# Kernel optimization log

Measured on AMD Instinct MI355X. Metric: run time of the kernel, lower is better.

The kernel has to match this reference:

```python
import jax, jax.numpy as jnp
import numpy as np

N_NODES = 50000
N_GRAPHS = 50
MAX_NODES = 1000  # equal-size graphs
C_IN = 128
C_OUT = 128
N_EDGES = 800000
N_LAYERS = 3
BN_EPS = 1e-5


def setup_inputs() -> dict:
    key = jax.random.key(0)
    ks = jax.random.split(key, 20)
    x = jax.random.normal(ks[0], (N_NODES, C_IN), dtype=jnp.float32)
    edge_index = jax.random.randint(ks[1], (2, N_EDGES), 0, N_NODES, dtype=jnp.int64)
    batch = jnp.repeat(jnp.arange(N_GRAPHS, dtype=jnp.int64), MAX_NODES)
    s_in = 1.0 / np.sqrt(C_IN)
    s_out = 1.0 / np.sqrt(C_OUT)
    fh_W = jax.random.normal(ks[2], (C_IN, C_OUT), dtype=jnp.float32) * s_in
    fh_b = jnp.zeros((C_OUT,), dtype=jnp.float32)
    W1 = jax.random.normal(ks[3], (N_LAYERS, C_OUT, C_OUT), dtype=jnp.float32) * s_out
    b1 = jnp.zeros((N_LAYERS, C_OUT), dtype=jnp.float32)
    g1 = jnp.ones((N_LAYERS, C_OUT), dtype=jnp.float32)
    be1 = jnp.zeros((N_LAYERS, C_OUT), dtype=jnp.float32)
    W2 = jax.random.normal(ks[4], (N_LAYERS, C_OUT, C_OUT), dtype=jnp.float32) * s_out
    b2 = jnp.zeros((N_LAYERS, C_OUT), dtype=jnp.float32)
    g2 = jnp.ones((N_LAYERS, C_OUT), dtype=jnp.float32)
    be2 = jnp.zeros((N_LAYERS, C_OUT), dtype=jnp.float32)
    return {"x": x, "edge_index": edge_index, "batch": batch,
            "fh_W": fh_W, "fh_b": fh_b,
            "W1": W1, "b1": b1, "g1": g1, "be1": be1,
            "W2": W2, "b2": b2, "g2": g2, "be2": be2}


def _bn(h, gamma, beta):
    # training-mode BatchNorm1d over the node dim (biased variance, like torch)
    mu = jnp.mean(h, axis=0)
    var = jnp.var(h, axis=0)
    return (h - mu) * jax.lax.rsqrt(var + BN_EPS) * gamma + beta


def _mlp(h, W1, b1, g1, be1, W2, b2, g2, be2):
    h = jax.nn.relu(_bn(h @ W1 + b1, g1, be1))
    h = jax.nn.relu(_bn(h @ W2 + b2, g2, be2))
    return h


def _to_dense_batch(h, batch):
    # counts per graph -> exclusive starts -> intra-graph position
    ones = jnp.ones((h.shape[0],), dtype=jnp.int32)
    counts = jax.ops.segment_sum(ones, batch, num_segments=N_GRAPHS)
    starts = jnp.cumsum(counts) - counts
    pos = jnp.arange(h.shape[0], dtype=jnp.int32) - starts[batch]
    dense = jnp.zeros((N_GRAPHS, MAX_NODES, h.shape[1]), dtype=h.dtype)
    return dense.at[batch, pos].set(h)


def reference(x, edge_index, batch, fh_W, fh_b, W1, b1, g1, be1, W2, b2, g2, be2):
    src, dst = edge_index[0], edge_index[1]
    h = x @ fh_W + fh_b  # first_head Linear
    outs = [_to_dense_batch(h, batch)]
    for l in range(N_LAYERS):
        # GINConv: mlp((1+eps)*x + sum_{j->i} x_j), eps=0
        agg = jax.ops.segment_sum(h[src], dst, num_segments=N_NODES)
        h = _mlp(h + agg, W1[l], b1[l], g1[l], be1[l], W2[l], b2[l], g2[l], be2[l])
        outs.append(_to_dense_batch(h, batch))
    return jnp.stack(outs)  # [N_LAYERS+1, B, MAX_NODES, C]
```

## Files before the change

### kernel.cpp

```cpp
#include <hip/hip_runtime.h>

#define NN 50000
#define NE 800000
#define CC 128
#define SLAB (NN * CC)
#define BN_EPS 1e-5f

typedef __attribute__((ext_vector_type(8))) short bf16x8;
typedef __attribute__((ext_vector_type(4))) float f32x4;
typedef unsigned short ushort_t;
typedef unsigned int uint_t;

__device__ inline ushort_t f2bf(float v) {
  unsigned u = __builtin_bit_cast(unsigned, v);
  unsigned r = u + 0x7FFFu + ((u >> 16) & 1u);
  return (ushort_t)(r >> 16);
}
__device__ inline float bf2f(unsigned lo16) { return __builtin_bit_cast(float, lo16 << 16); }

__global__ void zero_int_kernel(int* __restrict__ p, int n) {
  int i = blockIdx.x * blockDim.x + threadIdx.x;
  if (i < n) p[i] = 0;
}

__global__ void count_kernel(const int* __restrict__ dst, int* __restrict__ counts) {
  int e = blockIdx.x * blockDim.x + threadIdx.x;
  if (e < NE) atomicAdd(&counts[dst[e]], 1);
}

__global__ void scan1_kernel(const int* __restrict__ counts, int* __restrict__ excl,
                             int* __restrict__ blocksum) {
  __shared__ int s[256];
  int t = threadIdx.x;
  int i = blockIdx.x * 256 + t;
  int v = (i < NN) ? counts[i] : 0;
  s[t] = v;
  for (int off = 1; off < 256; off <<= 1) {
    __syncthreads();
    int add = (t >= off) ? s[t - off] : 0;
    __syncthreads();
    s[t] += add;
  }
  __syncthreads();
  if (i < NN) excl[i] = s[t] - v;
  if (t == 255) blocksum[blockIdx.x] = s[255];
}

__global__ void scan2_kernel(int* __restrict__ blocksum, int nb) {
  __shared__ int s[256];
  int t = threadIdx.x;
  int v = (t < nb) ? blocksum[t] : 0;
  s[t] = v;
  for (int off = 1; off < 256; off <<= 1) {
    __syncthreads();
    int add = (t >= off) ? s[t - off] : 0;
    __syncthreads();
    s[t] += add;
  }
  __syncthreads();
  if (t < nb) blocksum[t] = s[t] - v;
}

__global__ void scan3_kernel(int* __restrict__ excl, const int* __restrict__ blocksum) {
  int i = blockIdx.x * 256 + threadIdx.x;
  if (i < NN) excl[i] += blocksum[blockIdx.x];
}

__global__ void fill_kernel(const int* __restrict__ src, const int* __restrict__ dst,
                            const int* __restrict__ starts, int* __restrict__ fill,
                            int* __restrict__ bucket) {
  int e = blockIdx.x * blockDim.x + threadIdx.x;
  if (e < NE) {
    int d = dst[e];
    int pos = atomicAdd(&fill[d], 1);
    bucket[starts[d] + pos] = src[e];
  }
}

__global__ void prep_w_kernel(const float* __restrict__ fh_W, const float* __restrict__ W1,
                              const float* __restrict__ W2, short* __restrict__ whi,
                              short* __restrict__ wlo) {
  int m = blockIdx.x;
  const float* src = (m == 0) ? fh_W : ((m <= 3) ? W1 + (m - 1) * CC * CC : W2 + (m - 4) * CC * CC);
  short* hi = whi + m * CC * CC;
  short* lo = wlo + m * CC * CC;
  for (int it = 0; it < 64; ++it) {
    int idx = it * 256 + threadIdx.x;
    int j = idx & 7;
    int l = (idx >> 3) & 63;
    int nt = (idx >> 9) & 7;
    int ks = idx >> 12;
    int n = nt * 16 + (l & 15);
    int k = ks * 32 + ((l >> 4) << 3) + j;
    float v = src[k * CC + n];
    unsigned u = __builtin_bit_cast(unsigned, v);
    unsigned short h = (unsigned short)(u >> 16);
    float hf = __builtin_bit_cast(float, ((unsigned)h) << 16);
    float r = v - hf;
    unsigned ur = __builtin_bit_cast(unsigned, r);
    hi[idx] = (short)h;
    lo[idx] = (short)(ur >> 16);
  }
}

__global__ __launch_bounds__(256) void gemm0_kernel(
    const float* __restrict__ A, const short* __restrict__ Wp_hi, const short* __restrict__ Wp_lo,
    const float* __restrict__ bias, float* __restrict__ out, ushort_t* __restrict__ h16s) {
  const int t = threadIdx.x;
  const int l = t & 63;
  const int wv = t >> 6;
  const int m0 = blockIdx.x * 64 + wv * 16;
  const int row = m0 + (l & 15);
  const int kg = (l >> 4) * 8;

  f32x4 acc[8];
#pragma unroll
  for (int i = 0; i < 8; ++i) acc[i] = (f32x4){0.f, 0.f, 0.f, 0.f};

#pragma unroll
  for (int ks = 0; ks < 4; ++ks) {
    float av[8];
    if (row < NN) {
      const float* ap = &A[row * CC + ks * 32 + kg];
      float4 v0 = *(const float4*)ap;
      float4 v1 = *(const float4*)(ap + 4);
      av[0] = v0.x; av[1] = v0.y; av[2] = v0.z; av[3] = v0.w;
      av[4] = v1.x; av[5] = v1.y; av[6] = v1.z; av[7] = v1.w;
    } else {
#pragma unroll
      for (int i = 0; i < 8; ++i) av[i] = 0.f;
    }
    bf16x8 ah, al;
#pragma unroll
    for (int i = 0; i < 8; ++i) {
      unsigned u = __builtin_bit_cast(unsigned, av[i]);
      unsigned short hbits = (unsigned short)(u >> 16);
      float hf = __builtin_bit_cast(float, ((unsigned)hbits) << 16);
      float r = av[i] - hf;
      unsigned ur = __builtin_bit_cast(unsigned, r);
      ah[i] = (short)hbits;
      al[i] = (short)(ur >> 16);
    }
#pragma unroll
    for (int nt = 0; nt < 8; ++nt) {
      const int base = (ks * 8 + nt) * 512 + l * 8;
      bf16x8 wh = *(const bf16x8*)&Wp_hi[base];
      bf16x8 wl = *(const bf16x8*)&Wp_lo[base];
      acc[nt] = __builtin_amdgcn_mfma_f32_16x16x32_bf16(ah, wh, acc[nt], 0, 0, 0);
      acc[nt] = __builtin_amdgcn_mfma_f32_16x16x32_bf16(al, wh, acc[nt], 0, 0, 0);
      acc[nt] = __builtin_amdgcn_mfma_f32_16x16x32_bf16(ah, wl, acc[nt], 0, 0, 0);
    }
  }

  const int rbase = m0 + (l >> 4) * 4;
  const int cn = l & 15;
#pragma unroll
  for (int nt = 0; nt < 8; ++nt) {
    int c = nt * 16 + cn;
    float bv = bias[c];
#pragma unroll
    for (int r = 0; r < 4; ++r) {
      int rr = rbase + r;
      if (rr < NN) {
        float v = acc[nt][r] + bv;
        out[rr * CC + c] = v;
        h16s[(nt * NN + rr) * 16 + cn] = f2bf(v);
      }
    }
  }
}

__global__ __launch_bounds__(256) void gather_kernel(
    const ushort_t* __restrict__ h16s, const int* __restrict__ starts,
    const int* __restrict__ counts, const int* __restrict__ bucket,
    ushort_t* __restrict__ aggs) {
  const int slice = blockIdx.x & 7;
  const int t = threadIdx.x;
  const int g16 = t >> 4;
  const int lane16 = t & 15;
  const int j8 = lane16 & 7;
  const int half = lane16 >> 3;
  const int node = (blockIdx.x >> 3) * 16 + g16;
  const int wl_base = t & 48;
  const uint_t* tbl = (const uint_t*)h16s + slice * (NN * 8);

  float a0 = 0.f, a1 = 0.f;
  if (half == 0) {
    uint_t u = tbl[node * 8 + j8];
    a0 = bf2f(u & 0xFFFFu);
    a1 = bf2f(u >> 16);
  }
  const int s = starts[node];
  const int n = counts[node];
  for (int base = 0; base < n; base += 16) {
    int nb = n - base;
    if (nb > 16) nb = 16;
    int idx = (lane16 < nb) ? bucket[s + base + lane16] : -1;
#pragma unroll
    for (int k = 0; k < 8; ++k) {
      int sr = __shfl(idx, wl_base + 2 * k + half);
      if (sr >= 0) {
        uint_t u = tbl[sr * 8 + j8];
        a0 += bf2f(u & 0xFFFFu);
        a1 += bf2f(u >> 16);
      }
    }
  }
  a0 += __shfl_xor(a0, 8);
  a1 += __shfl_xor(a1, 8);
  if (half == 0) {
    ((uint_t*)aggs)[slice * (NN * 8) + node * 8 + j8] =
        (uint_t)f2bf(a0) | ((uint_t)f2bf(a1) << 16);
  }
}

__global__ __launch_bounds__(256) void gemm1_kernel(
    const ushort_t* __restrict__ aggs, const short* __restrict__ Wp_hi,
    const short* __restrict__ Wp_lo, const float* __restrict__ bias,
    ushort_t* __restrict__ tmp16, float* __restrict__ stats_out) {
  __shared__ float sred[2 * CC];
  const int t = threadIdx.x;
  const int l = t & 63;
  const int wv = t >> 6;
  const int m0 = blockIdx.x * 64 + wv * 16;
  const int row = m0 + (l & 15);
  const int kg = (l >> 4) * 8;
  sred[t] = 0.f;

  f32x4 acc[8];
#pragma unroll
  for (int i = 0; i < 8; ++i) acc[i] = (f32x4){0.f, 0.f, 0.f, 0.f};

#pragma unroll
  for (int ks = 0; ks < 4; ++ks) {
    const int ch0 = ks * 32 + kg;
    bf16x8 ah;
    if (row < NN) {
      ah = *(const bf16x8*)&aggs[((ch0 >> 4) * NN + row) * 16 + (ch0 & 15)];
    } else {
#pragma unroll
      for (int i = 0; i < 8; ++i) ah[i] = 0;
    }
#pragma unroll
    for (int nt = 0; nt < 8; ++nt) {
      const int base = (ks * 8 + nt) * 512 + l * 8;
      bf16x8 wh = *(const bf16x8*)&Wp_hi[base];
      bf16x8 wl = *(const bf16x8*)&Wp_lo[base];
      acc[nt] = __builtin_amdgcn_mfma_f32_16x16x32_bf16(ah, wh, acc[nt], 0, 0, 0);
      acc[nt] = __builtin_amdgcn_mfma_f32_16x16x32_bf16(ah, wl, acc[nt], 0, 0, 0);
    }
  }

  __syncthreads();
  const int rbase = m0 + (l >> 4) * 4;
  const int cn = l & 15;
#pragma unroll
  for (int nt = 0; nt < 8; ++nt) {
    int c = nt * 16 + cn;
    float bv = bias[c];
    float s = 0.f, qq = 0.f;
#pragma unroll
    for (int r = 0; r < 4; ++r) {
      int rr = rbase + r;
      if (rr < NN) {
        float v = acc[nt][r] + bv;
        tmp16[rr * CC + c] = f2bf(v);
        s += v; qq += v * v;
      }
    }
    s += __shfl_xor(s, 16); s += __shfl_xor(s, 32);
    qq += __shfl_xor(qq, 16); qq += __shfl_xor(qq, 32);
    if ((l >> 4) == 0) {
      atomicAdd(&sred[c], s);
      atomicAdd(&sred[CC + c], qq);
    }
  }
  __syncthreads();
  atomicAdd(&stats_out[t], sred[t]);
}

__global__ __launch_bounds__(256) void gemm2_kernel(
    ushort_t* __restrict__ tmp16, const short* __restrict__ Wp_hi,
    const short* __restrict__ Wp_lo, const float* __restrict__ bias,
    const float* __restrict__ stats_in, const float* __restrict__ g,
    const float* __restrict__ be, float* __restrict__ stats_out) {
  __shared__ float sred[2 * CC];
  const int t = threadIdx.x;
  const int l = t & 63;
  const int wv = t >> 6;
  const int m0 = blockIdx.x * 64 + wv * 16;
  const int row = m0 + (l & 15);
  const int kg = (l >> 4) * 8;
  sred[t] = 0.f;

  f32x4 acc[8];
#pragma unroll
  for (int i = 0; i < 8; ++i) acc[i] = (f32x4){0.f, 0.f, 0.f, 0.f};

#pragma unroll
  for (int ks = 0; ks < 4; ++ks) {
    bf16x8 ah;
    if (row < NN) {
      bf16x8 raw = *(const bf16x8*)&tmp16[row * CC + ks * 32 + kg];
#pragma unroll
      for (int i = 0; i < 8; ++i) {
        int c = ks * 32 + kg + i;
        float mu = stats_in[c] * (1.0f / NN);
        float var = fmaxf(stats_in[CC + c] * (1.0f / NN) - mu * mu, 0.f);
        float a = g[c] * rsqrtf(var + BN_EPS);
        float d = fmaf(-mu, a, be[c]);
        float v = bf2f((unsigned)(ushort_t)raw[i]);
        v = fmaxf(fmaf(v, a, d), 0.f);
        ah[i] = (short)f2bf(v);
      }
    } else {
#pragma unroll
      for (int i = 0; i < 8; ++i) ah[i] = 0;
    }
#pragma unroll
    for (int nt = 0; nt < 8; ++nt) {
      const int base = (ks * 8 + nt) * 512 + l * 8;
      bf16x8 wh = *(const bf16x8*)&Wp_hi[base];
      bf16x8 wl = *(const bf16x8*)&Wp_lo[base];
      acc[nt] = __builtin_amdgcn_mfma_f32_16x16x32_bf16(ah, wh, acc[nt], 0, 0, 0);
      acc[nt] = __builtin_amdgcn_mfma_f32_16x16x32_bf16(ah, wl, acc[nt], 0, 0, 0);
    }
  }

  __syncthreads();
  const int rbase = m0 + (l >> 4) * 4;
  const int cn = l & 15;
#pragma unroll
  for (int nt = 0; nt < 8; ++nt) {
    int c = nt * 16 + cn;
    float bv = bias[c];
    float s = 0.f, qq = 0.f;
#pragma unroll
    for (int r = 0; r < 4; ++r) {
      int rr = rbase + r;
      if (rr < NN) {
        float v = acc[nt][r] + bv;
        tmp16[rr * CC + c] = f2bf(v);
        s += v; qq += v * v;
      }
    }
    s += __shfl_xor(s, 16); s += __shfl_xor(s, 32);
    qq += __shfl_xor(qq, 16); qq += __shfl_xor(qq, 32);
    if ((l >> 4) == 0) {
      atomicAdd(&sred[c], s);
      atomicAdd(&sred[CC + c], qq);
    }
  }
  __syncthreads();
  atomicAdd(&stats_out[t], sred[t]);
}

__global__ __launch_bounds__(256) void apply_kernel(
    const ushort_t* __restrict__ t2, const float* __restrict__ stats2,
    const float* __restrict__ g2, const float* __restrict__ be2,
    float* __restrict__ outslab, ushort_t* __restrict__ h16s) {
  const int node = blockIdx.x * 256 + threadIdx.x;
  const int slice = blockIdx.y;
  if (node >= NN) return;
  const int c0 = slice * 16;

  const uint4* tp = (const uint4*)(t2 + node * CC + c0);
  uint4 r0 = tp[0], r1 = tp[1];
  unsigned w[4] = {r0.x, r0.y, r0.z, r0.w};
  unsigned w2[4] = {r1.x, r1.y, r1.z, r1.w};

  float vo[16];
#pragma unroll
  for (int j = 0; j < 8; ++j) {
    unsigned u = (j < 4) ? w[j] : w2[j - 4];
    vo[2 * j] = bf2f(u & 0xFFFFu);
    vo[2 * j + 1] = bf2f(u >> 16);
  }
#pragma unroll
  for (int j = 0; j < 16; ++j) {
    int c = c0 + j;
    float mu = stats2[c] * (1.0f / NN);
    float var = fmaxf(stats2[CC + c] * (1.0f / NN) - mu * mu, 0.f);
    float a = g2[c] * rsqrtf(var + BN_EPS);
    float d = fmaf(-mu, a, be2[c]);
    vo[j] = fmaxf(fmaf(vo[j], a, d), 0.f);
  }
  float* op = &outslab[node * CC + c0];
#pragma unroll
  for (int j = 0; j < 4; ++j) {
    float4 v = make_float4(vo[4 * j], vo[4 * j + 1], vo[4 * j + 2], vo[4 * j + 3]);
    *(float4*)&op[4 * j] = v;
  }
  if (h16s) {
    uint4 o0, o1;
    o0.x = (unsigned)f2bf(vo[0]) | ((unsigned)f2bf(vo[1]) << 16);
    o0.y = (unsigned)f2bf(vo[2]) | ((unsigned)f2bf(vo[3]) << 16);
    o0.z = (unsigned)f2bf(vo[4]) | ((unsigned)f2bf(vo[5]) << 16);
    o0.w = (unsigned)f2bf(vo[6]) | ((unsigned)f2bf(vo[7]) << 16);
    o1.x = (unsigned)f2bf(vo[8]) | ((unsigned)f2bf(vo[9]) << 16);
    o1.y = (unsigned)f2bf(vo[10]) | ((unsigned)f2bf(vo[11]) << 16);
    o1.z = (unsigned)f2bf(vo[12]) | ((unsigned)f2bf(vo[13]) << 16);
    o1.w = (unsigned)f2bf(vo[14]) | ((unsigned)f2bf(vo[15]) << 16);
    uint4* hp = (uint4*)(h16s + (slice * NN + node) * 16);
    hp[0] = o0;
    hp[1] = o1;
  }
}

extern "C" void kernel_launch(void* const* d_in, const int* in_sizes, int n_in,
                              void* d_out, int out_size, void* d_ws, size_t ws_size,
                              hipStream_t stream) {
  const float* x    = (const float*)d_in[0];
  const int*   edge = (const int*)d_in[1];
  const float* fh_W = (const float*)d_in[3];
  const float* fh_b = (const float*)d_in[4];
  const float* W1   = (const float*)d_in[5];
  const float* b1   = (const float*)d_in[6];
  const float* g1   = (const float*)d_in[7];
  const float* be1  = (const float*)d_in[8];
  const float* W2   = (const float*)d_in[9];
  const float* b2   = (const float*)d_in[10];
  const float* g2   = (const float*)d_in[11];
  const float* be2  = (const float*)d_in[12];
  float* out = (float*)d_out;

  const int* src = edge;
  const int* dst = edge + NE;

  int* counts   = (int*)d_ws;
  int* fill     = counts + 50048;
  float* stats  = (float*)(fill + 50048);
  int* starts   = (int*)(stats + 1536);
  int* blocksum = starts + 50048;
  int* bucket   = blocksum + 256;
  short* whi    = (short*)(bucket + NE);
  short* wlo    = whi + 7 * CC * CC;
  ushort_t* h16s = (ushort_t*)(wlo + 7 * CC * CC);
  ushort_t* aggs = h16s + SLAB;
  ushort_t* tmp16 = aggs + SLAB;

  zero_int_kernel<<<(101632 + 255) / 256, 256, 0, stream>>>(counts, 101632);
  count_kernel<<<NE / 256, 256, 0, stream>>>(dst, counts);
  scan1_kernel<<<196, 256, 0, stream>>>(counts, starts, blocksum);
  scan2_kernel<<<1, 256, 0, stream>>>(blocksum, 196);
  scan3_kernel<<<196, 256, 0, stream>>>(starts, blocksum);
  fill_kernel<<<NE / 256, 256, 0, stream>>>(src, dst, starts, fill, bucket);

  prep_w_kernel<<<7, 256, 0, stream>>>(fh_W, W1, W2, whi, wlo);

  gemm0_kernel<<<782, 256, 0, stream>>>(x, whi, wlo, fh_b, out, h16s);

  for (int ly = 0; ly < 3; ++ly) {
    float* stats1 = stats + (ly * 2) * 256;
    float* stats2 = stats + (ly * 2 + 1) * 256;
    gather_kernel<<<25000, 256, 0, stream>>>(h16s, starts, counts, bucket, aggs);
    gemm1_kernel<<<782, 256, 0, stream>>>(
        aggs, whi + (1 + ly) * CC * CC, wlo + (1 + ly) * CC * CC, b1 + ly * CC, tmp16, stats1);
    gemm2_kernel<<<782, 256, 0, stream>>>(
        tmp16, whi + (4 + ly) * CC * CC, wlo + (4 + ly) * CC * CC, b2 + ly * CC,
        stats1, g1 + ly * CC, be1 + ly * CC, stats2);
    apply_kernel<<<dim3(196, 8), 256, 0, stream>>>(
        tmp16, stats2, g2 + ly * CC, be2 + ly * CC, out + (ly + 1) * SLAB,
        (ly < 2) ? h16s : (ushort_t*)nullptr);
  }
}
```

Baseline: 571.8 us.

## Widen feature slices to 32 channels and batch independent gather loads per wave

The bf16 node-feature table changes from 8 slices of 16 channels to 4 slices of 32 channels, so each neighbor row fetch is 64 bytes instead of 32. The gather kernel now assigns one wave per node, with four neighbors handled in parallel per wave, and issues 8 (or 4) independent loads before accumulating to raise memory-level parallelism. The gemm0, gemm1 and apply kernels are updated to the new layout. The cost is a higher block count, extra tail-handling code, and more wasted lanes for nodes with few neighbors.

```diff
diff --git a/kernel.cpp b/kernel.cpp
--- a/kernel.cpp
+++ b/kernel.cpp
@@ -164,7 +164,7 @@
       if (rr < NN) {
         float v = acc[nt][r] + bv;
         out[rr * CC + c] = v;
-        h16s[(nt * NN + rr) * 16 + cn] = f2bf(v);
+        h16s[((c >> 5) * NN + rr) * 32 + (c & 31)] = f2bf(v);
       }
     }
   }
@@ -174,42 +174,69 @@
     const ushort_t* __restrict__ h16s, const int* __restrict__ starts,
     const int* __restrict__ counts, const int* __restrict__ bucket,
     ushort_t* __restrict__ aggs) {
-  const int slice = blockIdx.x & 7;
+  const int slice = blockIdx.x & 3;
   const int t = threadIdx.x;
-  const int g16 = t >> 4;
-  const int lane16 = t & 15;
-  const int j8 = lane16 & 7;
-  const int half = lane16 >> 3;
-  const int node = (blockIdx.x >> 3) * 16 + g16;
-  const int wl_base = t & 48;
-  const uint_t* tbl = (const uint_t*)h16s + slice * (NN * 8);
+  const int w = t >> 6;
+  const int l = t & 63;
+  const int q = l >> 4;
+  const int j16 = l & 15;
+  const int node = (blockIdx.x >> 2) * 4 + w;
+  const uint_t* tbl = (const uint_t*)h16s + slice * (NN * 16);
 
   float a0 = 0.f, a1 = 0.f;
-  if (half == 0) {
-    uint_t u = tbl[node * 8 + j8];
+  if (q == 0) {
+    uint_t u = tbl[node * 16 + j16];
     a0 = bf2f(u & 0xFFFFu);
     a1 = bf2f(u >> 16);
   }
   const int s = starts[node];
   const int n = counts[node];
-  for (int base = 0; base < n; base += 16) {
-    int nb = n - base;
-    if (nb > 16) nb = 16;
-    int idx = (lane16 < nb) ? bucket[s + base + lane16] : -1;
-#pragma unroll
-    for (int k = 0; k < 8; ++k) {
-      int sr = __shfl(idx, wl_base + 2 * k + half);
-      if (sr >= 0) {
-        uint_t u = tbl[sr * 8 + j8];
+  for (int base = 0; base < n; base += 64) {
+    int nb = min(n - base, 64);
+    int idx = (l < nb) ? bucket[s + base + l] : 0;
+    int jj = 0;
+    for (; jj + 32 <= nb; jj += 32) {
+      int sr[8];
+      uint_t u[8];
+#pragma unroll
+      for (int k = 0; k < 8; ++k) sr[k] = __shfl(idx, jj + 4 * k + q);
+#pragma unroll
+      for (int k = 0; k < 8; ++k) u[k] = tbl[sr[k] * 16 + j16];
+#pragma unroll
+      for (int k = 0; k < 8; ++k) {
+        a0 += bf2f(u[k] & 0xFFFFu);
+        a1 += bf2f(u[k] >> 16);
+      }
+    }
+    for (; jj + 16 <= nb; jj += 16) {
+      int sr[4];
+      uint_t u[4];
+#pragma unroll
+      for (int k = 0; k < 4; ++k) sr[k] = __shfl(idx, jj + 4 * k + q);
+#pragma unroll
+      for (int k = 0; k < 4; ++k) u[k] = tbl[sr[k] * 16 + j16];
+#pragma unroll
+      for (int k = 0; k < 4; ++k) {
+        a0 += bf2f(u[k] & 0xFFFFu);
+        a1 += bf2f(u[k] >> 16);
+      }
+    }
+    for (; jj < nb; jj += 4) {
+      int i = jj + q;
+      int sr = __shfl(idx, (i < nb) ? i : (nb - 1));
+      if (i < nb) {
+        uint_t u = tbl[sr * 16 + j16];
         a0 += bf2f(u & 0xFFFFu);
         a1 += bf2f(u >> 16);
       }
     }
   }
-  a0 += __shfl_xor(a0, 8);
-  a1 += __shfl_xor(a1, 8);
-  if (half == 0) {
-    ((uint_t*)aggs)[slice * (NN * 8) + node * 8 + j8] =
+  a0 += __shfl_xor(a0, 16);
+  a0 += __shfl_xor(a0, 32);
+  a1 += __shfl_xor(a1, 16);
+  a1 += __shfl_xor(a1, 32);
+  if (q == 0) {
+    ((uint_t*)aggs)[slice * (NN * 16) + node * 16 + j16] =
         (uint_t)f2bf(a0) | ((uint_t)f2bf(a1) << 16);
   }
 }
@@ -233,10 +260,9 @@
 
 #pragma unroll
   for (int ks = 0; ks < 4; ++ks) {
-    const int ch0 = ks * 32 + kg;
     bf16x8 ah;
     if (row < NN) {
-      ah = *(const bf16x8*)&aggs[((ch0 >> 4) * NN + row) * 16 + (ch0 & 15)];
+      ah = *(const bf16x8*)&aggs[(ks * NN + row) * 32 + kg];
     } else {
 #pragma unroll
       for (int i = 0; i < 8; ++i) ah[i] = 0;
@@ -362,22 +388,25 @@
   const int node = blockIdx.x * 256 + threadIdx.x;
   const int slice = blockIdx.y;
   if (node >= NN) return;
-  const int c0 = slice * 16;
+  const int c0 = slice * 32;
 
   const uint4* tp = (const uint4*)(t2 + node * CC + c0);
-  uint4 r0 = tp[0], r1 = tp[1];
-  unsigned w[4] = {r0.x, r0.y, r0.z, r0.w};
-  unsigned w2[4] = {r1.x, r1.y, r1.z, r1.w};
-
-  float vo[16];
-#pragma unroll
-  for (int j = 0; j < 8; ++j) {
-    unsigned u = (j < 4) ? w[j] : w2[j - 4];
-    vo[2 * j] = bf2f(u & 0xFFFFu);
-    vo[2 * j + 1] = bf2f(u >> 16);
-  }
-#pragma unroll
-  for (int j = 0; j < 16; ++j) {
+  uint4 r[4];
+#pragma unroll
+  for (int i = 0; i < 4; ++i) r[i] = tp[i];
+
+  float vo[32];
+#pragma unroll
+  for (int i = 0; i < 4; ++i) {
+    unsigned ws[4] = {r[i].x, r[i].y, r[i].z, r[i].w};
+#pragma unroll
+    for (int j = 0; j < 4; ++j) {
+      vo[i * 8 + 2 * j] = bf2f(ws[j] & 0xFFFFu);
+      vo[i * 8 + 2 * j + 1] = bf2f(ws[j] >> 16);
+    }
+  }
+#pragma unroll
+  for (int j = 0; j < 32; ++j) {
     int c = c0 + j;
     float mu = stats2[c] * (1.0f / NN);
     float var = fmaxf(stats2[CC + c] * (1.0f / NN) - mu * mu, 0.f);
@@ -387,23 +416,21 @@
   }
   float* op = &outslab[node * CC + c0];
 #pragma unroll
-  for (int j = 0; j < 4; ++j) {
+  for (int j = 0; j < 8; ++j) {
     float4 v = make_float4(vo[4 * j], vo[4 * j + 1], vo[4 * j + 2], vo[4 * j + 3]);
     *(float4*)&op[4 * j] = v;
   }
   if (h16s) {
-    uint4 o0, o1;
-    o0.x = (unsigned)f2bf(vo[0]) | ((unsigned)f2bf(vo[1]) << 16);
-    o0.y = (unsigned)f2bf(vo[2]) | ((unsigned)f2bf(vo[3]) << 16);
-    o0.z = (unsigned)f2bf(vo[4]) | ((unsigned)f2bf(vo[5]) << 16);
-    o0.w = (unsigned)f2bf(vo[6]) | ((unsigned)f2bf(vo[7]) << 16);
-    o1.x = (unsigned)f2bf(vo[8]) | ((unsigned)f2bf(vo[9]) << 16);
-    o1.y = (unsigned)f2bf(vo[10]) | ((unsigned)f2bf(vo[11]) << 16);
-    o1.z = (unsigned)f2bf(vo[12]) | ((unsigned)f2bf(vo[13]) << 16);
-    o1.w = (unsigned)f2bf(vo[14]) | ((unsigned)f2bf(vo[15]) << 16);
-    uint4* hp = (uint4*)(h16s + (slice * NN + node) * 16);
-    hp[0] = o0;
-    hp[1] = o1;
+    uint4* hp = (uint4*)(h16s + (slice * NN + node) * 32);
+#pragma unroll
+    for (int i = 0; i < 4; ++i) {
+      uint4 o;
+      o.x = (unsigned)f2bf(vo[i * 8 + 0]) | ((unsigned)f2bf(vo[i * 8 + 1]) << 16);
+      o.y = (unsigned)f2bf(vo[i * 8 + 2]) | ((unsigned)f2bf(vo[i * 8 + 3]) << 16);
+      o.z = (unsigned)f2bf(vo[i * 8 + 4]) | ((unsigned)f2bf(vo[i * 8 + 5]) << 16);
+      o.w = (unsigned)f2bf(vo[i * 8 + 6]) | ((unsigned)f2bf(vo[i * 8 + 7]) << 16);
+      hp[i] = o;
+    }
   }
 }
 
@@ -453,13 +480,13 @@
   for (int ly = 0; ly < 3; ++ly) {
     float* stats1 = stats + (ly * 2) * 256;
     float* stats2 = stats + (ly * 2 + 1) * 256;
-    gather_kernel<<<25000, 256, 0, stream>>>(h16s, starts, counts, bucket, aggs);
+    gather_kernel<<<50000, 256, 0, stream>>>(h16s, starts, counts, bucket, aggs);
     gemm1_kernel<<<782, 256, 0, stream>>>(
         aggs, whi + (1 + ly) * CC * CC, wlo + (1 + ly) * CC * CC, b1 + ly * CC, tmp16, stats1);
     gemm2_kernel<<<782, 256, 0, stream>>>(
         tmp16, whi + (4 + ly) * CC * CC, wlo + (4 + ly) * CC * CC, b2 + ly * CC,
         stats1, g1 + ly * CC, be1 + ly * CC, stats2);
-    apply_kernel<<<dim3(196, 8), 256, 0, stream>>>(
+    apply_kernel<<<dim3(196, 4), 256, 0, stream>>>(
         tmp16, stats2, g2 + ly * CC, be2 + ly * CC, out + (ly + 1) * SLAB,
         (ly < 2) ? h16s : (ushort_t*)nullptr);
   }
```

After: 596.0 us. 4.2% more time.
